# Optimization experiments

Hardware: AMD Instinct MI355X
Metric: run time of the kernel (lower is better)

Reference implementation:

```python
import jax, jax.numpy as jnp
import numpy as np
import math

LAMBDA_ATTRACT = 2.5
REPEL_STRENGTH = 0.15
EPSILON = 0.1  # repulsion distance offset
NORM_EPS = 1e-8
TAU_WEIGHT = 0.3
N = 8192


def _pairwise_angular(theta):
    # angular_distance(theta_i, theta_j) = min(|a-b|, 2*pi - |a-b|), shape [n, n]
    diff = jnp.abs(theta[:, None] - theta[None, :])
    return jnp.minimum(diff, 2.0 * math.pi - diff)


def setup_inputs() -> dict:
    key = jax.random.key(0)
    k1, k2 = jax.random.split(key)
    theta = jax.random.uniform(k1, (N,), dtype=jnp.float32, minval=-math.pi, maxval=math.pi)
    tau = jax.random.normal(k2, (N,), dtype=jnp.float32)
    return {"theta": theta, "tau": tau}


def reference(theta, tau):
    n = theta.shape[0]
    eye = jnp.eye(n, dtype=bool)

    d_theta = _pairwise_angular(theta)                      # [n, n]
    d_tau = jnp.abs(tau[:, None] - tau[None, :])            # [n, n]
    dist = d_theta + TAU_WEIGHT * d_tau

    # attention: exp(-lambda * dist), diagonal excluded, row-normalized
    dist_no_self = jnp.where(eye, jnp.inf, dist)
    scores = jnp.exp(-LAMBDA_ATTRACT * dist_no_self)
    attn = scores / jnp.sum(scores, axis=1, keepdims=True)

    cos_part = jnp.cos(theta)
    sin_part = jnp.sin(theta)
    R_x = attn @ cos_part
    R_y = attn @ sin_part

    # vectorized O(n^2) repulsion (replaces the python double loop)
    d = d_theta + EPSILON
    strength = REPEL_STRENGTH / (d * d)                     # [n, n]
    dx = cos_part[:, None] - cos_part[None, :]
    dy = sin_part[:, None] - sin_part[None, :]
    norm = jnp.sqrt(dx * dx + dy * dy) + NORM_EPS
    inv = jnp.where(eye, 0.0, strength / norm)              # mask i == j
    repel_force_x = jnp.sum(inv * dx, axis=1)
    repel_force_y = jnp.sum(inv * dy, axis=1)

    force_x = R_x + repel_force_x
    force_y = R_y + repel_force_y
    theta_out = jnp.arctan2(force_y, force_x)
    tau_out = attn @ tau
    return (theta_out, tau_out, attn)
```

## Files before the change

kernel.cpp:

```cpp
#include <hip/hip_runtime.h>
#include <math.h>

#define N_PTS 8192
#define TPB 256
#define RPB 4

__device__ inline float wave_reduce_sum(float v) {
    #pragma unroll
    for (int off = 32; off > 0; off >>= 1)
        v += __shfl_down(v, off, 64);
    return v;
}

__global__ void precompute_cs(const float* __restrict__ theta,
                              float* __restrict__ cs,
                              float* __restrict__ sn) {
    int i = blockIdx.x * blockDim.x + threadIdx.x;
    if (i < N_PTS) {
        float t = theta[i];
        cs[i] = cosf(t);
        sn[i] = sinf(t);
    }
}

__global__ __launch_bounds__(TPB) void geo_kernel(
    const float* __restrict__ theta,
    const float* __restrict__ tau,
    const float* __restrict__ cs,
    const float* __restrict__ sn,
    float* __restrict__ out)
{
    constexpr float LAMBDA   = 2.5f;
    constexpr float REPEL    = 0.15f;
    constexpr float EPS      = 0.1f;
    constexpr float NORM_EPS = 1e-8f;
    constexpr float TAUW     = 0.3f;
    constexpr float TWO_PI   = 6.28318530717958647692f;

    const int tid  = threadIdx.x;
    const int row0 = blockIdx.x * RPB;

    float* theta_out = out;
    float* tau_out   = out + N_PTS;
    float* attn      = out + 2 * N_PTS;

    float th_i[RPB], ta_i[RPB], c_i[RPB], s_i[RPB];
    #pragma unroll
    for (int r = 0; r < RPB; ++r) {
        th_i[r] = theta[row0 + r];
        ta_i[r] = tau[row0 + r];
        c_i[r]  = cs[row0 + r];
        s_i[r]  = sn[row0 + r];
    }

    float a_sum[RPB], a_x[RPB], a_y[RPB], a_t[RPB], rp_x[RPB], rp_y[RPB];
    #pragma unroll
    for (int r = 0; r < RPB; ++r) {
        a_sum[r] = 0.f; a_x[r] = 0.f; a_y[r] = 0.f;
        a_t[r]  = 0.f; rp_x[r] = 0.f; rp_y[r] = 0.f;
    }

    for (int j = tid; j < N_PTS; j += TPB) {
        float th_j = theta[j];
        float ta_j = tau[j];
        float c_j  = cs[j];
        float s_j  = sn[j];
        #pragma unroll
        for (int r = 0; r < RPB; ++r) {
            const int i = row0 + r;
            float diff = fabsf(th_i[r] - th_j);
            float dth  = fminf(diff, TWO_PI - diff);
            float dta  = fabsf(ta_i[r] - ta_j);
            float score = (j == i) ? 0.f : __expf(-LAMBDA * (dth + TAUW * dta));
            a_sum[r] += score;
            a_x[r]   += score * c_j;
            a_y[r]   += score * s_j;
            a_t[r]   += score * ta_j;
            float d   = dth + EPS;
            float dx  = c_i[r] - c_j;
            float dy  = s_i[r] - s_j;
            float nrm = sqrtf(dx * dx + dy * dy) + NORM_EPS;
            float inv = (j == i) ? 0.f : __fdividef(REPEL, d * d * nrm);
            rp_x[r] += inv * dx;
            rp_y[r] += inv * dy;
        }
    }

    __shared__ float red[RPB][6][TPB / 64];
    __shared__ float inv_s[RPB];
    const int wave = tid >> 6;
    const int lane = tid & 63;
    #pragma unroll
    for (int r = 0; r < RPB; ++r) {
        float v0 = wave_reduce_sum(a_sum[r]);
        float v1 = wave_reduce_sum(a_x[r]);
        float v2 = wave_reduce_sum(a_y[r]);
        float v3 = wave_reduce_sum(a_t[r]);
        float v4 = wave_reduce_sum(rp_x[r]);
        float v5 = wave_reduce_sum(rp_y[r]);
        if (lane == 0) {
            red[r][0][wave] = v0;
            red[r][1][wave] = v1;
            red[r][2][wave] = v2;
            red[r][3][wave] = v3;
            red[r][4][wave] = v4;
            red[r][5][wave] = v5;
        }
    }
    __syncthreads();

    if (tid < RPB) {
        const int r = tid;
        float s = 0.f, x = 0.f, y = 0.f, t = 0.f, rx = 0.f, ry = 0.f;
        #pragma unroll
        for (int w = 0; w < TPB / 64; ++w) {
            s  += red[r][0][w];
            x  += red[r][1][w];
            y  += red[r][2][w];
            t  += red[r][3][w];
            rx += red[r][4][w];
            ry += red[r][5][w];
        }
        float invsum = 1.0f / s;
        float fx = x * invsum + rx;
        float fy = y * invsum + ry;
        theta_out[row0 + r] = atan2f(fy, fx);
        tau_out[row0 + r]   = t * invsum;
        inv_s[r] = invsum;
    }
    __syncthreads();

    float invs[RPB];
    #pragma unroll
    for (int r = 0; r < RPB; ++r) invs[r] = inv_s[r];

    for (int j = tid; j < N_PTS; j += TPB) {
        float th_j = theta[j];
        float ta_j = tau[j];
        #pragma unroll
        for (int r = 0; r < RPB; ++r) {
            const int i = row0 + r;
            float diff = fabsf(th_i[r] - th_j);
            float dth  = fminf(diff, TWO_PI - diff);
            float dta  = fabsf(ta_i[r] - ta_j);
            float score = (j == i) ? 0.f : __expf(-LAMBDA * (dth + TAUW * dta));
            attn[(size_t)i * N_PTS + j] = score * invs[r];
        }
    }
}

extern "C" void kernel_launch(void* const* d_in, const int* in_sizes, int n_in,
                              void* d_out, int out_size, void* d_ws, size_t ws_size,
                              hipStream_t stream) {
    const float* theta = (const float*)d_in[0];
    const float* tau   = (const float*)d_in[1];
    float* cs  = (float*)d_ws;
    float* sn  = cs + N_PTS;
    float* out = (float*)d_out;

    precompute_cs<<<N_PTS / 256, 256, 0, stream>>>(theta, cs, sn);
    geo_kernel<<<N_PTS / RPB, TPB, 0, stream>>>(theta, tau, cs, sn, out);
}
```

Measured before the change: 332.0 us.

## Split into pack, reduction and attention-write kernels with branchless diagonal handling

Theta, tau, cos and sin are packed into float4/float2 arrays. The work is split into a reduction kernel and a separate attention-write kernel that launches one block per row. The diagonal branch is removed from the reduction loop: the self term is subtracted afterwards (score 1, self contributions), and the self repulsion vanishes because dx=dy=0. Exp uses exp2 with the normalization folded in as a log2 offset, the inner loops use hardware sqrt/rcp intrinsics with software prefetch, and the repel constant is hoisted. Risks are a small precision loss from the self-subtraction cancellation and the approximate intrinsics, plus extra launch overhead.

```diff
diff --git a/kernel.cpp b/kernel.cpp
--- a/kernel.cpp
+++ b/kernel.cpp
@@ -5,89 +5,111 @@
 #define TPB 256
 #define RPB 4
 
-__device__ inline float wave_reduce_sum(float v) {
+#define C_LAMBDA   2.5f
+#define C_REPEL    0.15f
+#define C_EPS      0.1f
+#define C_NORM_EPS 1e-8f
+#define C_TAUW     0.3f
+#define C_TWO_PI   6.28318530717958647692f
+#define C_NEG_L_LOG2E (-3.60673760222240625f)
+
+__device__ __forceinline__ float fast_exp2(float x) {
+#if __has_builtin(__builtin_amdgcn_exp2f)
+    return __builtin_amdgcn_exp2f(x);
+#else
+    return exp2f(x);
+#endif
+}
+__device__ __forceinline__ float fast_sqrt(float x) {
+#if __has_builtin(__builtin_amdgcn_sqrtf)
+    return __builtin_amdgcn_sqrtf(x);
+#else
+    return sqrtf(x);
+#endif
+}
+__device__ __forceinline__ float fast_rcp(float x) {
+#if __has_builtin(__builtin_amdgcn_rcpf)
+    return __builtin_amdgcn_rcpf(x);
+#else
+    return __fdividef(1.0f, x);
+#endif
+}
+__device__ __forceinline__ float fast_log2(float x) {
+#if __has_builtin(__builtin_amdgcn_logf)
+    return __builtin_amdgcn_logf(x);
+#else
+    return log2f(x);
+#endif
+}
+
+__device__ __forceinline__ float wave_reduce_sum(float v) {
     #pragma unroll
     for (int off = 32; off > 0; off >>= 1)
         v += __shfl_down(v, off, 64);
     return v;
 }
 
-__global__ void precompute_cs(const float* __restrict__ theta,
-                              float* __restrict__ cs,
-                              float* __restrict__ sn) {
+__global__ void pack_kernel(const float* __restrict__ theta,
+                            const float* __restrict__ tau,
+                            float4* __restrict__ pk,
+                            float2* __restrict__ pk2) {
     int i = blockIdx.x * blockDim.x + threadIdx.x;
-    if (i < N_PTS) {
-        float t = theta[i];
-        cs[i] = cosf(t);
-        sn[i] = sinf(t);
-    }
+    float t = theta[i];
+    float u = tau[i];
+    pk[i]  = make_float4(t, u, cosf(t), sinf(t));
+    pk2[i] = make_float2(t, u);
 }
 
-__global__ __launch_bounds__(TPB) void geo_kernel(
-    const float* __restrict__ theta,
-    const float* __restrict__ tau,
-    const float* __restrict__ cs,
-    const float* __restrict__ sn,
-    float* __restrict__ out)
+__global__ __launch_bounds__(TPB) void phase1_kernel(
+    const float4* __restrict__ pk,
+    float* __restrict__ out,
+    float* __restrict__ invsum)
 {
-    constexpr float LAMBDA   = 2.5f;
-    constexpr float REPEL    = 0.15f;
-    constexpr float EPS      = 0.1f;
-    constexpr float NORM_EPS = 1e-8f;
-    constexpr float TAUW     = 0.3f;
-    constexpr float TWO_PI   = 6.28318530717958647692f;
-
     const int tid  = threadIdx.x;
     const int row0 = blockIdx.x * RPB;
-
-    float* theta_out = out;
-    float* tau_out   = out + N_PTS;
-    float* attn      = out + 2 * N_PTS;
 
     float th_i[RPB], ta_i[RPB], c_i[RPB], s_i[RPB];
     #pragma unroll
     for (int r = 0; r < RPB; ++r) {
-        th_i[r] = theta[row0 + r];
-        ta_i[r] = tau[row0 + r];
-        c_i[r]  = cs[row0 + r];
-        s_i[r]  = sn[row0 + r];
+        float4 p = pk[row0 + r];
+        th_i[r] = p.x; ta_i[r] = p.y; c_i[r] = p.z; s_i[r] = p.w;
     }
 
     float a_sum[RPB], a_x[RPB], a_y[RPB], a_t[RPB], rp_x[RPB], rp_y[RPB];
     #pragma unroll
     for (int r = 0; r < RPB; ++r) {
         a_sum[r] = 0.f; a_x[r] = 0.f; a_y[r] = 0.f;
-        a_t[r]  = 0.f; rp_x[r] = 0.f; rp_y[r] = 0.f;
+        a_t[r] = 0.f; rp_x[r] = 0.f; rp_y[r] = 0.f;
     }
 
-    for (int j = tid; j < N_PTS; j += TPB) {
-        float th_j = theta[j];
-        float ta_j = tau[j];
-        float c_j  = cs[j];
-        float s_j  = sn[j];
+    float4 cur = pk[tid];
+    #pragma unroll 2
+    for (int k = 0; k < N_PTS / TPB; ++k) {
+        float4 nxt = pk[(tid + (k + 1) * TPB) & (N_PTS - 1)];
         #pragma unroll
         for (int r = 0; r < RPB; ++r) {
-            const int i = row0 + r;
-            float diff = fabsf(th_i[r] - th_j);
-            float dth  = fminf(diff, TWO_PI - diff);
-            float dta  = fabsf(ta_i[r] - ta_j);
-            float score = (j == i) ? 0.f : __expf(-LAMBDA * (dth + TAUW * dta));
+            float ad    = fabsf(th_i[r] - cur.x);
+            float dth   = fminf(ad, C_TWO_PI - ad);
+            float t     = fmaf(fabsf(ta_i[r] - cur.y), C_TAUW, dth);
+            float score = fast_exp2(t * C_NEG_L_LOG2E);
             a_sum[r] += score;
-            a_x[r]   += score * c_j;
-            a_y[r]   += score * s_j;
-            a_t[r]   += score * ta_j;
-            float d   = dth + EPS;
-            float dx  = c_i[r] - c_j;
-            float dy  = s_i[r] - s_j;
-            float nrm = sqrtf(dx * dx + dy * dy) + NORM_EPS;
-            float inv = (j == i) ? 0.f : __fdividef(REPEL, d * d * nrm);
-            rp_x[r] += inv * dx;
-            rp_y[r] += inv * dy;
+            a_x[r]   = fmaf(score, cur.z, a_x[r]);
+            a_y[r]   = fmaf(score, cur.w, a_y[r]);
+            a_t[r]   = fmaf(score, cur.y, a_t[r]);
+
+            float d   = dth + C_EPS;
+            float dx  = c_i[r] - cur.z;
+            float dy  = s_i[r] - cur.w;
+            float q   = fmaf(dx, dx, dy * dy);
+            float nrm = fast_sqrt(q) + C_NORM_EPS;
+            float inv = fast_rcp(d * d * nrm);
+            rp_x[r] = fmaf(inv, dx, rp_x[r]);
+            rp_y[r] = fmaf(inv, dy, rp_y[r]);
         }
+        cur = nxt;
     }
 
     __shared__ float red[RPB][6][TPB / 64];
-    __shared__ float inv_s[RPB];
     const int wave = tid >> 6;
     const int lane = tid & 63;
     #pragma unroll
@@ -99,12 +121,8 @@
         float v4 = wave_reduce_sum(rp_x[r]);
         float v5 = wave_reduce_sum(rp_y[r]);
         if (lane == 0) {
-            red[r][0][wave] = v0;
-            red[r][1][wave] = v1;
-            red[r][2][wave] = v2;
-            red[r][3][wave] = v3;
-            red[r][4][wave] = v4;
-            red[r][5][wave] = v5;
+            red[r][0][wave] = v0; red[r][1][wave] = v1; red[r][2][wave] = v2;
+            red[r][3][wave] = v3; red[r][4][wave] = v4; red[r][5][wave] = v5;
         }
     }
     __syncthreads();
@@ -114,38 +132,47 @@
         float s = 0.f, x = 0.f, y = 0.f, t = 0.f, rx = 0.f, ry = 0.f;
         #pragma unroll
         for (int w = 0; w < TPB / 64; ++w) {
-            s  += red[r][0][w];
-            x  += red[r][1][w];
-            y  += red[r][2][w];
-            t  += red[r][3][w];
-            rx += red[r][4][w];
-            ry += red[r][5][w];
+            s  += red[r][0][w]; x  += red[r][1][w]; y  += red[r][2][w];
+            t  += red[r][3][w]; rx += red[r][4][w]; ry += red[r][5][w];
         }
-        float invsum = 1.0f / s;
-        float fx = x * invsum + rx;
-        float fy = y * invsum + ry;
-        theta_out[row0 + r] = atan2f(fy, fx);
-        tau_out[row0 + r]   = t * invsum;
-        inv_s[r] = invsum;
+        float4 p = pk[row0 + r];
+        s -= 1.0f;
+        x -= p.z;
+        y -= p.w;
+        t -= p.y;
+        float invr = 1.0f / s;
+        float fx = fmaf(x, invr, C_REPEL * rx);
+        float fy = fmaf(y, invr, C_REPEL * ry);
+        out[row0 + r]         = atan2f(fy, fx);
+        out[N_PTS + row0 + r] = t * invr;
+        invsum[row0 + r]      = invr;
     }
-    __syncthreads();
+}
 
-    float invs[RPB];
-    #pragma unroll
-    for (int r = 0; r < RPB; ++r) invs[r] = inv_s[r];
+__global__ __launch_bounds__(TPB) void phase2_kernel(
+    const float2* __restrict__ pk2,
+    const float* __restrict__ invsum,
+    float* __restrict__ attn)
+{
+    const int i   = blockIdx.x;
+    const int tid = threadIdx.x;
+    float2 pi   = pk2[i];
+    float th_i  = pi.x;
+    float ta_i  = pi.y;
+    float l2inv = fast_log2(invsum[i]);
+    float* __restrict__ row = attn + (size_t)i * N_PTS;
 
-    for (int j = tid; j < N_PTS; j += TPB) {
-        float th_j = theta[j];
-        float ta_j = tau[j];
-        #pragma unroll
-        for (int r = 0; r < RPB; ++r) {
-            const int i = row0 + r;
-            float diff = fabsf(th_i[r] - th_j);
-            float dth  = fminf(diff, TWO_PI - diff);
-            float dta  = fabsf(ta_i[r] - ta_j);
-            float score = (j == i) ? 0.f : __expf(-LAMBDA * (dth + TAUW * dta));
-            attn[(size_t)i * N_PTS + j] = score * invs[r];
-        }
+    float2 cur = pk2[tid];
+    #pragma unroll 4
+    for (int k = 0; k < N_PTS / TPB; ++k) {
+        const int j = tid + k * TPB;
+        float2 nxt = pk2[(j + TPB) & (N_PTS - 1)];
+        float ad  = fabsf(th_i - cur.x);
+        float dth = fminf(ad, C_TWO_PI - ad);
+        float t   = fmaf(fabsf(ta_i - cur.y), C_TAUW, dth);
+        float v   = fast_exp2(fmaf(t, C_NEG_L_LOG2E, l2inv));
+        row[j] = (j == i) ? 0.0f : v;
+        cur = nxt;
     }
 }
 
@@ -154,10 +181,14 @@
                               hipStream_t stream) {
     const float* theta = (const float*)d_in[0];
     const float* tau   = (const float*)d_in[1];
-    float* cs  = (float*)d_ws;
-    float* sn  = cs + N_PTS;
-    float* out = (float*)d_out;
 
-    precompute_cs<<<N_PTS / 256, 256, 0, stream>>>(theta, cs, sn);
-    geo_kernel<<<N_PTS / RPB, TPB, 0, stream>>>(theta, tau, cs, sn, out);
+    float4* pk     = (float4*)d_ws;
+    float2* pk2    = (float2*)((char*)d_ws + 128 * 1024);
+    float*  invsum = (float*)((char*)d_ws + 192 * 1024);
+    float*  out    = (float*)d_out;
+    float*  attn   = out + 2 * N_PTS;
+
+    pack_kernel<<<N_PTS / 256, 256, 0, stream>>>(theta, tau, pk, pk2);
+    phase1_kernel<<<N_PTS / RPB, TPB, 0, stream>>>(pk, out, invsum);
+    phase2_kernel<<<N_PTS, TPB, 0, stream>>>(pk2, invsum, attn);
 }
```

New measurement: 299.9 us. 9.7% less time.
